# Kernel tuning notes

Measured on AMD Instinct MI355X. Metric: run time of the kernel, lower is better.

Reference implementation:

```python
import jax, jax.numpy as jnp
import numpy as np

# biased_softplus(1.0): bias chosen so softplus(bias) == 1.0 (tensordict NormalParamExtractor default)
_SP_BIAS = float(np.log(np.expm1(1.0)))  # ~0.5413
_SCALE_LB = 1e-4


def setup_inputs() -> dict:
    key = jax.random.key(0)
    ks = jax.random.split(key, 8)
    N, E = 100000, 1600000
    x = jax.random.normal(ks[0], (N, 27), dtype=jnp.float32)
    edge_index = jax.random.randint(ks[1], (2, E), 0, N, dtype=jnp.int64)
    # Linear(27, 64)
    W1 = jax.random.normal(ks[2], (27, 64), dtype=jnp.float32) * 0.1
    b1 = jnp.zeros((64,), dtype=jnp.float32)
    # GraphConv(64, 64): lin_rel (with bias) applied to aggregated neighbors, lin_root (no bias) to self
    Wrel = jax.random.normal(ks[3], (64, 64), dtype=jnp.float32) * 0.1
    brel = jnp.zeros((64,), dtype=jnp.float32)
    Wroot = jax.random.normal(ks[4], (64, 64), dtype=jnp.float32) * 0.1
    # Linear(64, 16)
    W2 = jax.random.normal(ks[5], (64, 16), dtype=jnp.float32) * 0.1
    b2 = jnp.zeros((16,), dtype=jnp.float32)
    return {"x": x, "edge_index": edge_index, "W1": W1, "b1": b1,
            "Wrel": Wrel, "brel": brel, "Wroot": Wroot, "W2": W2, "b2": b2}


def reference(x, edge_index, W1, b1, Wrel, brel, Wroot, W2, b2):
    N = x.shape[0]
    # Linear(27 -> 64)
    h = x @ W1 + b1  # [N, 64]
    # GraphConv: out = lin_rel(sum_{j in N(i)} h_j) + lin_root(h_i)
    src, dst = edge_index[0], edge_index[1]
    agg = jax.ops.segment_sum(h[src], dst, num_segments=N)  # [N, 64]
    h = agg @ Wrel + brel + h @ Wroot
    h = jnp.tanh(h)
    # Linear(64 -> 16) + Tanh
    o = jnp.tanh(h @ W2 + b2)  # [N, 16]
    # NormalParamExtractor: split in half, biased softplus on scale
    loc, raw_scale = jnp.split(o, 2, axis=-1)  # each [N, 8]
    scale = jnp.clip(jax.nn.softplus(raw_scale + _SP_BIAS), _SCALE_LB, None)
    # non-list branch: loc.t().squeeze(-1), scale.t().squeeze(-1)
    return loc.T, scale.T  # each [8, N]
```

## Files before the change

### kernel.cpp

```cpp
#include <hip/hip_runtime.h>
#include <hip/hip_bf16.h>
#include <math.h>

typedef unsigned short ushort_t;
typedef float f32x4 __attribute__((ext_vector_type(4)));
typedef short bf16x8v __attribute__((ext_vector_type(8)));

static constexpr float SP_BIAS = 0.5413248546129181f;
#define LB   512
#define LCAP 12288
#define PCAP 16384
#define MAXB 256
#define CHK  2048
#define BEPB 8192
#define SCAP 96
#define XP   32

__device__ __forceinline__ ushort_t f2bf(float f) {
    union { float f; unsigned u; } v; v.f = f;
    unsigned r = v.u + 0x7FFFu + ((v.u >> 16) & 1u);
    return (ushort_t)(r >> 16);
}
__device__ __forceinline__ float hi2f(unsigned u) {
    union { unsigned u; float f; } v; v.u = u & 0xFFFF0000u;
    return v.f;
}
__device__ __forceinline__ float lo2f(unsigned u) {
    union { unsigned u; float f; } v; v.u = u << 16;
    return v.f;
}

__global__ __launch_bounds__(256) void k_front(
        const int* __restrict__ ei, int* __restrict__ bucketArr,
        int* __restrict__ cellCnt, int E, int NB, int GBIN,
        const float* __restrict__ x, ushort_t* __restrict__ x_bf,
        int N, int GCVT, int* __restrict__ dummyIdx,
        const float* __restrict__ W1, const float* __restrict__ b1,
        const float* __restrict__ Wrel, const float* __restrict__ brel,
        const float* __restrict__ Wroot, const float* __restrict__ W2,
        ushort_t* __restrict__ wF, ushort_t* __restrict__ w2F,
        float* __restrict__ baV, float* __restrict__ bbV) {
    __shared__ alignas(16) char smem[(MAXB + 2 * CHK) * 4];
    __shared__ int s_flag;
    int bid = blockIdx.x, tid = threadIdx.x;
    if (bid < GBIN) {
        int* cursor = (int*)smem;
        int* s_dst  = cursor + MAXB;
        int* s_src  = s_dst + CHK;
        if (tid == 0) s_flag = 0;
        for (int i = tid; i < NB; i += 256) cursor[i] = 0;
        __syncthreads();
        int blk0 = bid * BEPB;
        {
            int cnt0 = E - blk0; if (cnt0 > CHK) cnt0 = CHK;
            int found = 0;
            for (int i = tid; i < cnt0; i += 256) {
                if (ei[2 * (blk0 + i) + 1] != 0) { found = 1; break; }
            }
            if (found) atomicOr(&s_flag, 1);
        }
        __syncthreads();
        int mode32 = s_flag;
        for (int ch = 0; ch < 4; ++ch) {
            int e0 = blk0 + ch * CHK;
            if (e0 >= E) break;
            int cnt = E - e0; if (cnt > CHK) cnt = CHK;
            if (mode32) {
                if ((E & 3) == 0) {
                    const int4* ps = (const int4*)(ei + e0);
                    const int4* pd = (const int4*)(ei + E + e0);
                    int nv = cnt >> 2;
                    for (int i = tid; i < nv; i += 256) {
                        ((int4*)s_src)[i] = ps[i];
                        ((int4*)s_dst)[i] = pd[i];
                    }
                    for (int i = (nv << 2) + tid; i < cnt; i += 256) {
                        s_src[i] = ei[e0 + i];
                        s_dst[i] = ei[E + e0 + i];
                    }
                } else {
                    for (int i = tid; i < cnt; i += 256) {
                        s_src[i] = ei[e0 + i];
                        s_dst[i] = ei[E + e0 + i];
                    }
                }
            } else {
                if ((E & 1) == 0) {
                    const uint4* ps = (const uint4*)ei + (e0 >> 1);
                    const uint4* pd = (const uint4*)ei + ((E + e0) >> 1);
                    int nv = cnt >> 1;
                    for (int i = tid; i < nv; i += 256) {
                        uint4 s = ps[i], d = pd[i];
                        s_src[2 * i] = (int)s.x; s_src[2 * i + 1] = (int)s.z;
                        s_dst[2 * i] = (int)d.x; s_dst[2 * i + 1] = (int)d.z;
                    }
                    if ((cnt & 1) && tid == 0) {
                        s_src[cnt - 1] = ei[2 * (e0 + cnt - 1)];
                        s_dst[cnt - 1] = ei[2 * (E + e0 + cnt - 1)];
                    }
                } else {
                    const int2* p = (const int2*)ei;
                    for (int i = tid; i < cnt; i += 256) {
                        s_src[i] = p[e0 + i].x;
                        s_dst[i] = p[E + e0 + i].x;
                    }
                }
            }
            __syncthreads();
            for (int i = tid; i < cnt; i += 256) {
                int d = s_dst[i];
                int b = d >> 9;
                int pos = atomicAdd(&cursor[b], 1);
                if (pos < SCAP)
                    bucketArr[((size_t)b * GBIN + bid) * SCAP + pos] =
                        ((d & 511) << 17) | s_src[i];
            }
            __syncthreads();
        }
        for (int b = tid; b < NB; b += 256) {
            int cc = cursor[b];
            if (cc > SCAP) cc = SCAP;
            cellCnt[(size_t)bid * NB + b] = cc;
        }
    } else if (bid < GBIN + GCVT) {
        int base = (bid - GBIN) * 64;
        int row = base + (tid >> 2);
        if (row <= N) {
            int c0 = (tid & 3) * 8;
            ushort_t o[8];
#pragma unroll
            for (int c = 0; c < 8; ++c) {
                int col = c0 + c;
                float v = (row < N && col < 27) ? x[(size_t)row * 27 + col] : 0.f;
                o[c] = f2bf(v);
            }
            *(uint4*)(x_bf + (size_t)row * XP + c0) = *(const uint4*)o;
        }
    } else {
        int wb = bid - GBIN - GCVT;
        if (wb < 2) {
            const float* Wr = (wb == 0) ? Wrel : Wroot;
            for (int e = tid; e < 2048; e += 256) {
                int j = e & 7, lane = (e >> 3) & 63, nt = e >> 9;
                int k = ((lane >> 4) << 3) + j;
                int n = (nt << 4) + (lane & 15);
                float v = 0.f;
                if (k < 27) {
                    for (int m = 0; m < 64; ++m)
                        v = fmaf(W1[k * 64 + m], Wr[m * 64 + n], v);
                }
                wF[wb * 2048 + e] = f2bf(v);
            }
        } else {
            for (int e = tid; e < 1024; e += 256) {
                int j = e & 7, lane = (e >> 3) & 63, kt = e >> 9;
                int k = (kt << 5) + ((lane >> 4) << 3) + j;
                int n = (lane & 15);
                w2F[e] = f2bf(W2[k * 16 + n]);
            }
            if (tid < 64) {
                float a = 0.f, b = 0.f;
                for (int m = 0; m < 64; ++m) {
                    a = fmaf(b1[m], Wrel[m * 64 + tid], a);
                    b = fmaf(b1[m], Wroot[m * 64 + tid], b);
                }
                baV[tid] = a;
                bbV[tid] = b + brel[tid];
            }
            if (tid == 255) *dummyIdx = N;
        }
    }
}

__global__ __launch_bounds__(256) void k_local(const int* __restrict__ bucketArr,
                                               const int* __restrict__ cellCnt,
                                               int GBIN, int NB,
                                               int* __restrict__ src_padded,
                                               int* __restrict__ pstart,
                                               int* __restrict__ pdeg,
                                               int* __restrict__ degN,
                                               int N) {
    __shared__ int hist[LB];
    __shared__ int ppos[LB];
    __shared__ int cursor[LB];
    __shared__ int sdata[256];
    __shared__ alignas(16) int spad[LCAP];
    int b = blockIdx.x, tid = threadIdx.x;
    for (int i = tid; i < LB; i += 256) hist[i] = 0;
    __syncthreads();
    const int* arr = bucketArr + (size_t)b * GBIN * SCAP;
    for (int c = tid; c < GBIN; c += 256) {
        const int4* cell4 = (const int4*)(arr + (size_t)c * SCAP);
        int cc = cellCnt[(size_t)c * NB + b];
        int nq = (cc + 3) >> 2;
        for (int q = 0; q < nq; ++q) {
            int4 v = cell4[q];
            int b4 = q * 4;
            if (b4 + 0 < cc) atomicAdd(&hist[v.x >> 17], 1);
            if (b4 + 1 < cc) atomicAdd(&hist[v.y >> 17], 1);
            if (b4 + 2 < cc) atomicAdd(&hist[v.z >> 17], 1);
            if (b4 + 3 < cc) atomicAdd(&hist[v.w >> 17], 1);
        }
    }
    __syncthreads();
    int v0 = hist[2 * tid], v1 = hist[2 * tid + 1];
    int p0 = (v0 + 1) & ~1, p1 = (v1 + 1) & ~1;
    int psum = p0 + p1;
    sdata[tid] = psum;
    __syncthreads();
    for (int off = 1; off < 256; off <<= 1) {
        int add = (tid >= off) ? sdata[tid - off] : 0;
        __syncthreads();
        sdata[tid] += add;
        __syncthreads();
    }
    int pexcl = sdata[tid] - psum;
    ppos[2 * tid] = pexcl;          cursor[2 * tid] = pexcl;
    ppos[2 * tid + 1] = pexcl + p0; cursor[2 * tid + 1] = pexcl + p0;
    __syncthreads();
    int ptot = sdata[255];
    int ptotR = (ptot + 3) & ~3;
    if (ptotR > LCAP) ptotR = LCAP;
    for (int i = tid; i < ptotR; i += 256) spad[i] = N;
    __syncthreads();
    for (int c = tid; c < GBIN; c += 256) {
        const int4* cell4 = (const int4*)(arr + (size_t)c * SCAP);
        int cc = cellCnt[(size_t)c * NB + b];
        int nq = (cc + 3) >> 2;
        for (int q = 0; q < nq; ++q) {
            int4 v = cell4[q];
            int b4 = q * 4;
            int e[4] = {v.x, v.y, v.z, v.w};
#pragma unroll
            for (int r = 0; r < 4; ++r) {
                if (b4 + r < cc) {
                    int pk = e[r];
                    int pos = atomicAdd(&cursor[pk >> 17], 1);
                    if (pos < LCAP) spad[pos] = pk & 0x1FFFF;
                }
            }
        }
    }
    __syncthreads();
    int* outp = src_padded + (size_t)b * PCAP;
    int nt4 = ptotR >> 2;
    for (int i = tid; i < nt4; i += 256)
        ((int4*)outp)[i] = ((const int4*)spad)[i];
    int n0 = b * LB;
    for (int ln = tid; ln < LB; ln += 256) {
        int node = n0 + ln;
        if (node < N) {
            pstart[node] = b * PCAP + ppos[ln];
            pdeg[node] = (hist[ln] + 1) & ~1;
            degN[node] = hist[ln];
        }
    }
}

__global__ __launch_bounds__(256) void k_agg(const ushort_t* __restrict__ x_bf,
                                             const int* __restrict__ src_padded,
                                             const int* __restrict__ pstart,
                                             const int* __restrict__ pdeg,
                                             const int* __restrict__ dummyIdx,
                                             ushort_t* __restrict__ aggx_bf, int N) {
    int w = (blockIdx.x * 256 + threadIdx.x) >> 6;
    int t = threadIdx.x & 63;
    int base = w * 8;
    if (base >= N) return;
    int sub = t >> 3, off = t & 7;
    int node = base + sub;
    int ok = (node < N);
    int st = ok ? pstart[node] : 0;
    int nr = ok ? pdeg[node] : 0;
    const int* ip = src_padded + st;
    int nrmax = nr;
    nrmax = max(nrmax, __shfl_xor(nrmax, 8));
    nrmax = max(nrmax, __shfl_xor(nrmax, 16));
    nrmax = max(nrmax, __shfl_xor(nrmax, 32));
    float a0 = 0.f, a1 = 0.f, a2 = 0.f, a3 = 0.f;
    for (int k = 0; k < nrmax; k += 8) {
        const int* q0 = (k     < nr) ? ip + k     : dummyIdx;
        const int* q1 = (k     < nr) ? ip + k + 1 : dummyIdx;
        const int* q2 = (k + 2 < nr) ? ip + k + 2 : dummyIdx;
        const int* q3 = (k + 2 < nr) ? ip + k + 3 : dummyIdx;
        const int* q4 = (k + 4 < nr) ? ip + k + 4 : dummyIdx;
        const int* q5 = (k + 4 < nr) ? ip + k + 5 : dummyIdx;
        const int* q6 = (k + 6 < nr) ? ip + k + 6 : dummyIdx;
        const int* q7 = (k + 6 < nr) ? ip + k + 7 : dummyIdx;
        int r0 = *q0, r1 = *q1, r2 = *q2, r3 = *q3;
        int r4 = *q4, r5 = *q5, r6 = *q6, r7 = *q7;
        uint2 u0 = *(const uint2*)(x_bf + (size_t)r0 * XP + off * 4);
        uint2 u1 = *(const uint2*)(x_bf + (size_t)r1 * XP + off * 4);
        uint2 u2 = *(const uint2*)(x_bf + (size_t)r2 * XP + off * 4);
        uint2 u3 = *(const uint2*)(x_bf + (size_t)r3 * XP + off * 4);
        uint2 u4 = *(const uint2*)(x_bf + (size_t)r4 * XP + off * 4);
        uint2 u5 = *(const uint2*)(x_bf + (size_t)r5 * XP + off * 4);
        uint2 u6 = *(const uint2*)(x_bf + (size_t)r6 * XP + off * 4);
        uint2 u7 = *(const uint2*)(x_bf + (size_t)r7 * XP + off * 4);
        a0 += lo2f(u0.x); a1 += hi2f(u0.x); a2 += lo2f(u0.y); a3 += hi2f(u0.y);
        a0 += lo2f(u1.x); a1 += hi2f(u1.x); a2 += lo2f(u1.y); a3 += hi2f(u1.y);
        a0 += lo2f(u2.x); a1 += hi2f(u2.x); a2 += lo2f(u2.y); a3 += hi2f(u2.y);
        a0 += lo2f(u3.x); a1 += hi2f(u3.x); a2 += lo2f(u3.y); a3 += hi2f(u3.y);
        a0 += lo2f(u4.x); a1 += hi2f(u4.x); a2 += lo2f(u4.y); a3 += hi2f(u4.y);
        a0 += lo2f(u5.x); a1 += hi2f(u5.x); a2 += lo2f(u5.y); a3 += hi2f(u5.y);
        a0 += lo2f(u6.x); a1 += hi2f(u6.x); a2 += lo2f(u6.y); a3 += hi2f(u6.y);
        a0 += lo2f(u7.x); a1 += hi2f(u7.x); a2 += lo2f(u7.y); a3 += hi2f(u7.y);
    }
    if (ok) {
        uint2 d;
        d.x = ((unsigned)f2bf(a1) << 16) | f2bf(a0);
        d.y = ((unsigned)f2bf(a3) << 16) | f2bf(a2);
        *(uint2*)(aggx_bf + (size_t)node * XP + off * 4) = d;
    }
}

__global__ __launch_bounds__(256) void k_tail(const ushort_t* __restrict__ x_bf,
                                              const ushort_t* __restrict__ aggx_bf,
                                              const int* __restrict__ degN,
                                              const ushort_t* __restrict__ wF_g,
                                              const ushort_t* __restrict__ w2F_g,
                                              const float* __restrict__ baV,
                                              const float* __restrict__ bbV,
                                              const float* __restrict__ b2,
                                              float* __restrict__ out,
                                              int N, int ntiles) {
    __shared__ alignas(16) ushort_t WF[8 * 512];
    __shared__ alignas(16) ushort_t W2F[2 * 512];
    __shared__ alignas(16) ushort_t h2T[4][16 * 72];
    __shared__ float baS[64];
    __shared__ float bbS[64];
    __shared__ float b2S[16];
    int tid = threadIdx.x;
    for (int i = tid; i < 512; i += 256) ((uint4*)WF)[i] = ((const uint4*)wF_g)[i];
    for (int i = tid; i < 128; i += 256) ((uint4*)W2F)[i] = ((const uint4*)w2F_g)[i];
    if (tid < 64) { baS[tid] = baV[tid]; bbS[tid] = bbV[tid]; }
    if (tid < 16) b2S[tid] = b2[tid];
    __syncthreads();

    int lane = tid & 63;
    int wv = tid >> 6;
    int lrow = lane & 15;
    int lkg = lane >> 4;
    const bf16x8v* WFV  = (const bf16x8v*)WF;
    const bf16x8v* W2V  = (const bf16x8v*)W2F;
    ushort_t* myT = h2T[wv];

    for (int tile = blockIdx.x * 4 + wv; tile < ntiles; tile += gridDim.x * 4) {
        int rbase = tile * 16;
        int arow = rbase + lrow; if (arow >= N) arow = N - 1;
        const bf16x8v* aggV = (const bf16x8v*)(aggx_bf + (size_t)arow * XP);
        const bf16x8v* xV   = (const bf16x8v*)(x_bf + (size_t)arow * XP);
        bf16x8v a0 = aggV[lkg];
        bf16x8v a1 = xV[lkg];

        f32x4 acc[4];
#pragma unroll
        for (int nt = 0; nt < 4; ++nt) { acc[nt] = (f32x4){0.f, 0.f, 0.f, 0.f}; }
#pragma unroll
        for (int nt = 0; nt < 4; ++nt) {
            acc[nt] = __builtin_amdgcn_mfma_f32_16x16x32_bf16(a0, WFV[(0 * 4 + nt) * 64 + lane], acc[nt], 0, 0, 0);
            acc[nt] = __builtin_amdgcn_mfma_f32_16x16x32_bf16(a1, WFV[(1 * 4 + nt) * 64 + lane], acc[nt], 0, 0, 0);
        }
        float dgv[4];
#pragma unroll
        for (int r = 0; r < 4; ++r) {
            int node = rbase + lkg * 4 + r;
            dgv[r] = (node < N) ? (float)degN[node] : 0.f;
        }
#pragma unroll
        for (int nt = 0; nt < 4; ++nt) {
            int feat = nt * 16 + lrow;
            float ba = baS[feat], bb = bbS[feat];
#pragma unroll
            for (int r = 0; r < 4; ++r) {
                int noderow = lkg * 4 + r;
                float val = acc[nt][r] + bb + dgv[r] * ba;
                myT[noderow * 72 + feat] = f2bf(tanhf(val));
            }
        }
        __threadfence_block();
        const bf16x8v* h2V = (const bf16x8v*)myT;
        bf16x8v p0 = h2V[lrow * 9 + lkg];
        bf16x8v p1 = h2V[lrow * 9 + 4 + lkg];
        f32x4 acc2 = (f32x4){0.f, 0.f, 0.f, 0.f};
        acc2 = __builtin_amdgcn_mfma_f32_16x16x32_bf16(p0, W2V[0 * 64 + lane], acc2, 0, 0, 0);
        acc2 = __builtin_amdgcn_mfma_f32_16x16x32_bf16(p1, W2V[1 * 64 + lane], acc2, 0, 0, 0);

        int feat = lrow;
        float bias2 = b2S[feat];
#pragma unroll
        for (int r = 0; r < 4; ++r) {
            int node = rbase + lkg * 4 + r;
            float o = tanhf(acc2[r] + bias2);
            if (feat >= 8) {
                float sp = log1pf(expf(o + SP_BIAS));
                o = fmaxf(sp, 1e-4f);
            }
            if (node < N) out[(size_t)feat * N + node] = o;
        }
        __threadfence_block();
    }
}

extern "C" void kernel_launch(void* const* d_in, const int* in_sizes, int n_in,
                              void* d_out, int out_size, void* d_ws, size_t ws_size,
                              hipStream_t stream) {
    const float* x    = (const float*)d_in[0];
    const int*   ei   = (const int*)d_in[1];
    const float* W1   = (const float*)d_in[2];
    const float* b1   = (const float*)d_in[3];
    const float* Wrel = (const float*)d_in[4];
    const float* brel = (const float*)d_in[5];
    const float* Wroot= (const float*)d_in[6];
    const float* W2   = (const float*)d_in[7];
    const float* b2   = (const float*)d_in[8];

    int N = in_sizes[0] / 27;
    int E = in_sizes[1] / 2;

    int NB = (N + LB - 1) / LB;
    int GBIN = (E + BEPB - 1) / BEPB;
    int GCVT = (N + 64) / 64;

    ushort_t* x_bf       = (ushort_t*)d_ws;
    ushort_t* aggx_bf    = x_bf + (size_t)(N + 1) * XP;
    ushort_t* wF_g       = aggx_bf + (size_t)N * XP;
    ushort_t* w2F_g      = wF_g + 4096;
    float*    baV        = (float*)(w2F_g + 1024);
    float*    bbV        = baV + 64;
    int*      bucketArr  = (int*)(bbV + 64);
    int*      cellCnt    = bucketArr + (size_t)NB * GBIN * SCAP;
    int*      src_padded = cellCnt + (size_t)GBIN * NB;
    int*      pstart     = src_padded + (size_t)NB * PCAP;
    int*      pdeg       = pstart + N;
    int*      degN       = pdeg + N;
    int*      dummyIdx   = degN + N;

    int ntiles16 = (N + 15) / 16;

    k_front<<<GBIN + GCVT + 3, 256, 0, stream>>>(
        ei, bucketArr, cellCnt, E, NB, GBIN,
        x, x_bf, N, GCVT, dummyIdx,
        W1, b1, Wrel, brel, Wroot, W2, wF_g, w2F_g, baV, bbV);
    k_local<<<NB, 256, 0, stream>>>(bucketArr, cellCnt, GBIN, NB, src_padded,
                                    pstart, pdeg, degN, N);
    int nwaves8 = (N + 7) / 8;
    k_agg<<<(nwaves8 + 3) / 4, 256, 0, stream>>>(x_bf, src_padded, pstart, pdeg,
                                                 dummyIdx, aggx_bf, N);
    int tgrid = (ntiles16 + 3) / 4; if (tgrid > 1024) tgrid = 1024;
    k_tail<<<tgrid, 256, 0, stream>>>(x_bf, aggx_bf, degN, wF_g, w2F_g,
                                      baV, bbV, b2, (float*)d_out, N, ntiles16);
}
```

Baseline: 80.85 us.

## Stream edges directly into bucket scatter and parallelize cell reads across threads

The binning stage now scatters edges straight from global loads, with no shared-memory staging and no chunk barriers. Each block covers twice as many edges, with larger per-cell capacity, so there are fewer binning blocks. The local sort kernel caches cell counts in shared memory and spreads (cell, quad) work items over all threads, rather than having one thread walk a whole cell serially, which improves load balance and memory parallelism. In exchange, fewer blocks run in the front kernel, bucket storage grows with the larger SCAP, and overflow clipping depends on the new capacity.

Measured after the change: 82.69 us. +2.3%, slower.

```diff
diff --git a/kernel.cpp b/kernel.cpp
--- a/kernel.cpp
+++ b/kernel.cpp
@@ -11,9 +11,9 @@
 #define LCAP 12288
 #define PCAP 16384
 #define MAXB 256
-#define CHK  2048
-#define BEPB 8192
-#define SCAP 96
+#define BEPB 16384
+#define SCAP 160
+#define MAXG 384
 #define XP   32
 
 __device__ __forceinline__ ushort_t f2bf(float f) {
@@ -40,83 +40,67 @@
         const float* __restrict__ Wroot, const float* __restrict__ W2,
         ushort_t* __restrict__ wF, ushort_t* __restrict__ w2F,
         float* __restrict__ baV, float* __restrict__ bbV) {
-    __shared__ alignas(16) char smem[(MAXB + 2 * CHK) * 4];
+    __shared__ int cursor[MAXB];
     __shared__ int s_flag;
     int bid = blockIdx.x, tid = threadIdx.x;
     if (bid < GBIN) {
-        int* cursor = (int*)smem;
-        int* s_dst  = cursor + MAXB;
-        int* s_src  = s_dst + CHK;
         if (tid == 0) s_flag = 0;
         for (int i = tid; i < NB; i += 256) cursor[i] = 0;
         __syncthreads();
         int blk0 = bid * BEPB;
+        int cnt = E - blk0; if (cnt > BEPB) cnt = BEPB;
         {
-            int cnt0 = E - blk0; if (cnt0 > CHK) cnt0 = CHK;
+            int nchk = cnt < 2048 ? cnt : 2048;
             int found = 0;
-            for (int i = tid; i < cnt0; i += 256) {
+            for (int i = tid; i < nchk; i += 256) {
                 if (ei[2 * (blk0 + i) + 1] != 0) { found = 1; break; }
             }
             if (found) atomicOr(&s_flag, 1);
         }
         __syncthreads();
         int mode32 = s_flag;
-        for (int ch = 0; ch < 4; ++ch) {
-            int e0 = blk0 + ch * CHK;
-            if (e0 >= E) break;
-            int cnt = E - e0; if (cnt > CHK) cnt = CHK;
-            if (mode32) {
-                if ((E & 3) == 0) {
-                    const int4* ps = (const int4*)(ei + e0);
-                    const int4* pd = (const int4*)(ei + E + e0);
-                    int nv = cnt >> 2;
-                    for (int i = tid; i < nv; i += 256) {
-                        ((int4*)s_src)[i] = ps[i];
-                        ((int4*)s_dst)[i] = pd[i];
-                    }
-                    for (int i = (nv << 2) + tid; i < cnt; i += 256) {
-                        s_src[i] = ei[e0 + i];
-                        s_dst[i] = ei[E + e0 + i];
-                    }
-                } else {
-                    for (int i = tid; i < cnt; i += 256) {
-                        s_src[i] = ei[e0 + i];
-                        s_dst[i] = ei[E + e0 + i];
-                    }
+        auto scat = [&](int src, int dst) {
+            int b = dst >> 9;
+            int pos = atomicAdd(&cursor[b], 1);
+            if (pos < SCAP)
+                bucketArr[((size_t)b * GBIN + bid) * SCAP + pos] =
+                    ((dst & 511) << 17) | src;
+        };
+        if (mode32) {
+            if ((E & 3) == 0) {
+                const int4* ps = (const int4*)(ei + blk0);
+                const int4* pd = (const int4*)(ei + E + blk0);
+                int nv = cnt >> 2;
+                for (int i = tid; i < nv; i += 256) {
+                    int4 s = ps[i], d = pd[i];
+                    scat(s.x, d.x); scat(s.y, d.y);
+                    scat(s.z, d.z); scat(s.w, d.w);
                 }
+                for (int i = (nv << 2) + tid; i < cnt; i += 256)
+                    scat(ei[blk0 + i], ei[E + blk0 + i]);
             } else {
-                if ((E & 1) == 0) {
-                    const uint4* ps = (const uint4*)ei + (e0 >> 1);
-                    const uint4* pd = (const uint4*)ei + ((E + e0) >> 1);
-                    int nv = cnt >> 1;
-                    for (int i = tid; i < nv; i += 256) {
-                        uint4 s = ps[i], d = pd[i];
-                        s_src[2 * i] = (int)s.x; s_src[2 * i + 1] = (int)s.z;
-                        s_dst[2 * i] = (int)d.x; s_dst[2 * i + 1] = (int)d.z;
-                    }
-                    if ((cnt & 1) && tid == 0) {
-                        s_src[cnt - 1] = ei[2 * (e0 + cnt - 1)];
-                        s_dst[cnt - 1] = ei[2 * (E + e0 + cnt - 1)];
-                    }
-                } else {
-                    const int2* p = (const int2*)ei;
-                    for (int i = tid; i < cnt; i += 256) {
-                        s_src[i] = p[e0 + i].x;
-                        s_dst[i] = p[E + e0 + i].x;
-                    }
+                for (int i = tid; i < cnt; i += 256)
+                    scat(ei[blk0 + i], ei[E + blk0 + i]);
+            }
+        } else {
+            if ((E & 1) == 0) {
+                const uint4* ps = (const uint4*)ei + (blk0 >> 1);
+                const uint4* pd = (const uint4*)ei + ((E + blk0) >> 1);
+                int nv = cnt >> 1;
+                for (int i = tid; i < nv; i += 256) {
+                    uint4 s = ps[i], d = pd[i];
+                    scat((int)s.x, (int)d.x);
+                    scat((int)s.z, (int)d.z);
                 }
-            }
-            __syncthreads();
-            for (int i = tid; i < cnt; i += 256) {
-                int d = s_dst[i];
-                int b = d >> 9;
-                int pos = atomicAdd(&cursor[b], 1);
-                if (pos < SCAP)
-                    bucketArr[((size_t)b * GBIN + bid) * SCAP + pos] =
-                        ((d & 511) << 17) | s_src[i];
-            }
-            __syncthreads();
-        }
+                if ((cnt & 1) && tid == 0)
+                    scat(ei[2 * (blk0 + cnt - 1)], ei[2 * (E + blk0 + cnt - 1)]);
+            } else {
+                const int2* p = (const int2*)ei;
+                for (int i = tid; i < cnt; i += 256)
+                    scat(p[blk0 + i].x, p[E + blk0 + i].x);
+            }
+        }
+        __syncthreads();
         for (int b = tid; b < NB; b += 256) {
             int cc = cursor[b];
             if (cc > SCAP) cc = SCAP;
@@ -184,23 +168,25 @@
     __shared__ int ppos[LB];
     __shared__ int cursor[LB];
     __shared__ int sdata[256];
+    __shared__ int ccnt[MAXG];
     __shared__ alignas(16) int spad[LCAP];
     int b = blockIdx.x, tid = threadIdx.x;
     for (int i = tid; i < LB; i += 256) hist[i] = 0;
+    for (int i = tid; i < GBIN; i += 256) ccnt[i] = cellCnt[(size_t)i * NB + b];
     __syncthreads();
     const int* arr = bucketArr + (size_t)b * GBIN * SCAP;
-    for (int c = tid; c < GBIN; c += 256) {
-        const int4* cell4 = (const int4*)(arr + (size_t)c * SCAP);
-        int cc = cellCnt[(size_t)c * NB + b];
-        int nq = (cc + 3) >> 2;
-        for (int q = 0; q < nq; ++q) {
-            int4 v = cell4[q];
-            int b4 = q * 4;
-            if (b4 + 0 < cc) atomicAdd(&hist[v.x >> 17], 1);
-            if (b4 + 1 < cc) atomicAdd(&hist[v.y >> 17], 1);
-            if (b4 + 2 < cc) atomicAdd(&hist[v.z >> 17], 1);
-            if (b4 + 3 < cc) atomicAdd(&hist[v.w >> 17], 1);
-        }
+    const int QPC = SCAP >> 2;
+    int items = GBIN * QPC;
+    for (int i = tid; i < items; i += 256) {
+        int c = i / QPC, q = i - c * QPC;
+        int cc = ccnt[c];
+        int b4 = q * 4;
+        if (b4 >= cc) continue;
+        int4 v = ((const int4*)(arr + (size_t)c * SCAP))[q];
+        atomicAdd(&hist[v.x >> 17], 1);
+        if (b4 + 1 < cc) atomicAdd(&hist[v.y >> 17], 1);
+        if (b4 + 2 < cc) atomicAdd(&hist[v.z >> 17], 1);
+        if (b4 + 3 < cc) atomicAdd(&hist[v.w >> 17], 1);
     }
     __syncthreads();
     int v0 = hist[2 * tid], v1 = hist[2 * tid + 1];
@@ -223,21 +209,19 @@
     if (ptotR > LCAP) ptotR = LCAP;
     for (int i = tid; i < ptotR; i += 256) spad[i] = N;
     __syncthreads();
-    for (int c = tid; c < GBIN; c += 256) {
-        const int4* cell4 = (const int4*)(arr + (size_t)c * SCAP);
-        int cc = cellCnt[(size_t)c * NB + b];
-        int nq = (cc + 3) >> 2;
-        for (int q = 0; q < nq; ++q) {
-            int4 v = cell4[q];
-            int b4 = q * 4;
-            int e[4] = {v.x, v.y, v.z, v.w};
-#pragma unroll
-            for (int r = 0; r < 4; ++r) {
-                if (b4 + r < cc) {
-                    int pk = e[r];
-                    int pos = atomicAdd(&cursor[pk >> 17], 1);
-                    if (pos < LCAP) spad[pos] = pk & 0x1FFFF;
-                }
+    for (int i = tid; i < items; i += 256) {
+        int c = i / QPC, q = i - c * QPC;
+        int cc = ccnt[c];
+        int b4 = q * 4;
+        if (b4 >= cc) continue;
+        int4 v = ((const int4*)(arr + (size_t)c * SCAP))[q];
+        int e[4] = {v.x, v.y, v.z, v.w};
+#pragma unroll
+        for (int r = 0; r < 4; ++r) {
+            if (b4 + r < cc) {
+                int pk = e[r];
+                int pos = atomicAdd(&cursor[pk >> 17], 1);
+                if (pos < LCAP) spad[pos] = pk & 0x1FFFF;
             }
         }
     }
```

## Fuse local bucket sort with neighbor aggregation, gathering from shared-memory CSR

Applied to the files above, without the earlier changes.

Merges the per-bucket local sort kernel and the aggregation kernel into one. Each block now gathers neighbor features using the source indices it has just placed in shared memory, so it no longer writes and re-reads src_padded, pstart and pdeg in global memory, and one launch goes away. The histogram and scatter loops are also flattened to one work item per cell quad, with cell counts cached in shared memory, and the shared buffer is shrunk. In exchange, the gather phase runs on only about NB (~196) blocks instead of thousands, which may leave too few waves to hide gather latency. The smaller shared-memory capacity also raises the risk of overflow when a bucket is dense.

After: 98.23 us. 1.21x slower.

```diff
diff --git a/kernel.cpp b/kernel.cpp
--- a/kernel.cpp
+++ b/kernel.cpp
@@ -7,14 +7,14 @@
 typedef short bf16x8v __attribute__((ext_vector_type(8)));
 
 static constexpr float SP_BIAS = 0.5413248546129181f;
-#define LB   512
-#define LCAP 12288
-#define PCAP 16384
-#define MAXB 256
-#define CHK  2048
-#define BEPB 8192
-#define SCAP 96
-#define XP   32
+#define LB    512
+#define LCAP2 10240
+#define MAXB  256
+#define CHK   2048
+#define BEPB  8192
+#define SCAP  96
+#define MAXG  256
+#define XP    32
 
 __device__ __forceinline__ ushort_t f2bf(float f) {
     union { float f; unsigned u; } v; v.f = f;
@@ -34,7 +34,7 @@
         const int* __restrict__ ei, int* __restrict__ bucketArr,
         int* __restrict__ cellCnt, int E, int NB, int GBIN,
         const float* __restrict__ x, ushort_t* __restrict__ x_bf,
-        int N, int GCVT, int* __restrict__ dummyIdx,
+        int N, int GCVT,
         const float* __restrict__ W1, const float* __restrict__ b1,
         const float* __restrict__ Wrel, const float* __restrict__ brel,
         const float* __restrict__ Wroot, const float* __restrict__ W2,
@@ -167,40 +167,40 @@
                 baV[tid] = a;
                 bbV[tid] = b + brel[tid];
             }
-            if (tid == 255) *dummyIdx = N;
-        }
-    }
-}
-
-__global__ __launch_bounds__(256) void k_local(const int* __restrict__ bucketArr,
-                                               const int* __restrict__ cellCnt,
-                                               int GBIN, int NB,
-                                               int* __restrict__ src_padded,
-                                               int* __restrict__ pstart,
-                                               int* __restrict__ pdeg,
-                                               int* __restrict__ degN,
-                                               int N) {
+        }
+    }
+}
+
+__global__ __launch_bounds__(256) void k_locagg(const int* __restrict__ bucketArr,
+                                                const int* __restrict__ cellCnt,
+                                                int GBIN, int NB,
+                                                const ushort_t* __restrict__ x_bf,
+                                                ushort_t* __restrict__ aggx_bf,
+                                                int* __restrict__ degN,
+                                                int N) {
     __shared__ int hist[LB];
     __shared__ int ppos[LB];
     __shared__ int cursor[LB];
     __shared__ int sdata[256];
-    __shared__ alignas(16) int spad[LCAP];
+    __shared__ int ccnt[MAXG];
+    __shared__ alignas(16) int spad[LCAP2];
     int b = blockIdx.x, tid = threadIdx.x;
     for (int i = tid; i < LB; i += 256) hist[i] = 0;
+    for (int i = tid; i < GBIN; i += 256) ccnt[i] = cellCnt[(size_t)i * NB + b];
     __syncthreads();
     const int* arr = bucketArr + (size_t)b * GBIN * SCAP;
-    for (int c = tid; c < GBIN; c += 256) {
-        const int4* cell4 = (const int4*)(arr + (size_t)c * SCAP);
-        int cc = cellCnt[(size_t)c * NB + b];
-        int nq = (cc + 3) >> 2;
-        for (int q = 0; q < nq; ++q) {
-            int4 v = cell4[q];
-            int b4 = q * 4;
-            if (b4 + 0 < cc) atomicAdd(&hist[v.x >> 17], 1);
-            if (b4 + 1 < cc) atomicAdd(&hist[v.y >> 17], 1);
-            if (b4 + 2 < cc) atomicAdd(&hist[v.z >> 17], 1);
-            if (b4 + 3 < cc) atomicAdd(&hist[v.w >> 17], 1);
-        }
+    const int QPC = SCAP >> 2;
+    int items = GBIN * QPC;
+    for (int i = tid; i < items; i += 256) {
+        int c = i / QPC, q = i - c * QPC;
+        int cc = ccnt[c];
+        int b4 = q * 4;
+        if (b4 >= cc) continue;
+        int4 v = ((const int4*)(arr + (size_t)c * SCAP))[q];
+        atomicAdd(&hist[v.x >> 17], 1);
+        if (b4 + 1 < cc) atomicAdd(&hist[v.y >> 17], 1);
+        if (b4 + 2 < cc) atomicAdd(&hist[v.z >> 17], 1);
+        if (b4 + 3 < cc) atomicAdd(&hist[v.w >> 17], 1);
     }
     __syncthreads();
     int v0 = hist[2 * tid], v1 = hist[2 * tid + 1];
@@ -220,97 +220,78 @@
     __syncthreads();
     int ptot = sdata[255];
     int ptotR = (ptot + 3) & ~3;
-    if (ptotR > LCAP) ptotR = LCAP;
+    if (ptotR > LCAP2) ptotR = LCAP2;
     for (int i = tid; i < ptotR; i += 256) spad[i] = N;
     __syncthreads();
-    for (int c = tid; c < GBIN; c += 256) {
-        const int4* cell4 = (const int4*)(arr + (size_t)c * SCAP);
-        int cc = cellCnt[(size_t)c * NB + b];
-        int nq = (cc + 3) >> 2;
-        for (int q = 0; q < nq; ++q) {
-            int4 v = cell4[q];
-            int b4 = q * 4;
-            int e[4] = {v.x, v.y, v.z, v.w};
-#pragma unroll
-            for (int r = 0; r < 4; ++r) {
-                if (b4 + r < cc) {
-                    int pk = e[r];
-                    int pos = atomicAdd(&cursor[pk >> 17], 1);
-                    if (pos < LCAP) spad[pos] = pk & 0x1FFFF;
-                }
-            }
-        }
-    }
-    __syncthreads();
-    int* outp = src_padded + (size_t)b * PCAP;
-    int nt4 = ptotR >> 2;
-    for (int i = tid; i < nt4; i += 256)
-        ((int4*)outp)[i] = ((const int4*)spad)[i];
+    for (int i = tid; i < items; i += 256) {
+        int c = i / QPC, q = i - c * QPC;
+        int cc = ccnt[c];
+        int b4 = q * 4;
+        if (b4 >= cc) continue;
+        int4 v = ((const int4*)(arr + (size_t)c * SCAP))[q];
+        int e[4] = {v.x, v.y, v.z, v.w};
+#pragma unroll
+        for (int r = 0; r < 4; ++r) {
+            if (b4 + r < cc) {
+                int pk = e[r];
+                int pos = atomicAdd(&cursor[pk >> 17], 1);
+                if (pos < LCAP2) spad[pos] = pk & 0x1FFFF;
+            }
+        }
+    }
+    __syncthreads();
     int n0 = b * LB;
+    int lane = tid & 63, wv = tid >> 6;
+    int sub = lane >> 3, off = lane & 7;
+    for (int it = 0; it < LB / 32; ++it) {
+        int ln = it * 32 + wv * 8 + sub;
+        int node = n0 + ln;
+        int ok = (node < N);
+        int pp = ppos[ln];
+        int h = hist[ln];
+        int nr = ok ? ((h + 1) & ~1) : 0;
+        int nrmax = nr;
+        nrmax = max(nrmax, __shfl_xor(nrmax, 8));
+        nrmax = max(nrmax, __shfl_xor(nrmax, 16));
+        nrmax = max(nrmax, __shfl_xor(nrmax, 32));
+        float a0 = 0.f, a1 = 0.f, a2 = 0.f, a3 = 0.f;
+        for (int k = 0; k < nrmax; k += 8) {
+            int r0 = (k     < nr) ? spad[pp + k]     : N;
+            int r1 = (k     < nr) ? spad[pp + k + 1] : N;
+            int r2 = (k + 2 < nr) ? spad[pp + k + 2] : N;
+            int r3 = (k + 2 < nr) ? spad[pp + k + 3] : N;
+            int r4 = (k + 4 < nr) ? spad[pp + k + 4] : N;
+            int r5 = (k + 4 < nr) ? spad[pp + k + 5] : N;
+            int r6 = (k + 6 < nr) ? spad[pp + k + 6] : N;
+            int r7 = (k + 6 < nr) ? spad[pp + k + 7] : N;
+            uint2 u0 = *(const uint2*)(x_bf + (size_t)r0 * XP + off * 4);
+            uint2 u1 = *(const uint2*)(x_bf + (size_t)r1 * XP + off * 4);
+            uint2 u2 = *(const uint2*)(x_bf + (size_t)r2 * XP + off * 4);
+            uint2 u3 = *(const uint2*)(x_bf + (size_t)r3 * XP + off * 4);
+            uint2 u4 = *(const uint2*)(x_bf + (size_t)r4 * XP + off * 4);
+            uint2 u5 = *(const uint2*)(x_bf + (size_t)r5 * XP + off * 4);
+            uint2 u6 = *(const uint2*)(x_bf + (size_t)r6 * XP + off * 4);
+            uint2 u7 = *(const uint2*)(x_bf + (size_t)r7 * XP + off * 4);
+            a0 += lo2f(u0.x); a1 += hi2f(u0.x); a2 += lo2f(u0.y); a3 += hi2f(u0.y);
+            a0 += lo2f(u1.x); a1 += hi2f(u1.x); a2 += lo2f(u1.y); a3 += hi2f(u1.y);
+            a0 += lo2f(u2.x); a1 += hi2f(u2.x); a2 += lo2f(u2.y); a3 += hi2f(u2.y);
+            a0 += lo2f(u3.x); a1 += hi2f(u3.x); a2 += lo2f(u3.y); a3 += hi2f(u3.y);
+            a0 += lo2f(u4.x); a1 += hi2f(u4.x); a2 += lo2f(u4.y); a3 += hi2f(u4.y);
+            a0 += lo2f(u5.x); a1 += hi2f(u5.x); a2 += lo2f(u5.y); a3 += hi2f(u5.y);
+            a0 += lo2f(u6.x); a1 += hi2f(u6.x); a2 += lo2f(u6.y); a3 += hi2f(u6.y);
+            a0 += lo2f(u7.x); a1 += hi2f(u7.x); a2 += lo2f(u7.y); a3 += hi2f(u7.y);
+        }
+        if (ok) {
+            uint2 d;
+            d.x = ((unsigned)f2bf(a1) << 16) | f2bf(a0);
+            d.y = ((unsigned)f2bf(a3) << 16) | f2bf(a2);
+            *(uint2*)(aggx_bf + (size_t)node * XP + off * 4) = d;
+            if (lane < 8) {  }
+        }
+    }
     for (int ln = tid; ln < LB; ln += 256) {
         int node = n0 + ln;
-        if (node < N) {
-            pstart[node] = b * PCAP + ppos[ln];
-            pdeg[node] = (hist[ln] + 1) & ~1;
-            degN[node] = hist[ln];
-        }
-    }
-}
-
-__global__ __launch_bounds__(256) void k_agg(const ushort_t* __restrict__ x_bf,
-                                             const int* __restrict__ src_padded,
-                                             const int* __restrict__ pstart,
-                                             const int* __restrict__ pdeg,
-                                             const int* __restrict__ dummyIdx,
-                                             ushort_t* __restrict__ aggx_bf, int N) {
-    int w = (blockIdx.x * 256 + threadIdx.x) >> 6;
-    int t = threadIdx.x & 63;
-    int base = w * 8;
-    if (base >= N) return;
-    int sub = t >> 3, off = t & 7;
-    int node = base + sub;
-    int ok = (node < N);
-    int st = ok ? pstart[node] : 0;
-    int nr = ok ? pdeg[node] : 0;
-    const int* ip = src_padded + st;
-    int nrmax = nr;
-    nrmax = max(nrmax, __shfl_xor(nrmax, 8));
-    nrmax = max(nrmax, __shfl_xor(nrmax, 16));
-    nrmax = max(nrmax, __shfl_xor(nrmax, 32));
-    float a0 = 0.f, a1 = 0.f, a2 = 0.f, a3 = 0.f;
-    for (int k = 0; k < nrmax; k += 8) {
-        const int* q0 = (k     < nr) ? ip + k     : dummyIdx;
-        const int* q1 = (k     < nr) ? ip + k + 1 : dummyIdx;
-        const int* q2 = (k + 2 < nr) ? ip + k + 2 : dummyIdx;
-        const int* q3 = (k + 2 < nr) ? ip + k + 3 : dummyIdx;
-        const int* q4 = (k + 4 < nr) ? ip + k + 4 : dummyIdx;
-        const int* q5 = (k + 4 < nr) ? ip + k + 5 : dummyIdx;
-        const int* q6 = (k + 6 < nr) ? ip + k + 6 : dummyIdx;
-        const int* q7 = (k + 6 < nr) ? ip + k + 7 : dummyIdx;
-        int r0 = *q0, r1 = *q1, r2 = *q2, r3 = *q3;
-        int r4 = *q4, r5 = *q5, r6 = *q6, r7 = *q7;
-        uint2 u0 = *(const uint2*)(x_bf + (size_t)r0 * XP + off * 4);
-        uint2 u1 = *(const uint2*)(x_bf + (size_t)r1 * XP + off * 4);
-        uint2 u2 = *(const uint2*)(x_bf + (size_t)r2 * XP + off * 4);
-        uint2 u3 = *(const uint2*)(x_bf + (size_t)r3 * XP + off * 4);
-        uint2 u4 = *(const uint2*)(x_bf + (size_t)r4 * XP + off * 4);
-        uint2 u5 = *(const uint2*)(x_bf + (size_t)r5 * XP + off * 4);
-        uint2 u6 = *(const uint2*)(x_bf + (size_t)r6 * XP + off * 4);
-        uint2 u7 = *(const uint2*)(x_bf + (size_t)r7 * XP + off * 4);
-        a0 += lo2f(u0.x); a1 += hi2f(u0.x); a2 += lo2f(u0.y); a3 += hi2f(u0.y);
-        a0 += lo2f(u1.x); a1 += hi2f(u1.x); a2 += lo2f(u1.y); a3 += hi2f(u1.y);
-        a0 += lo2f(u2.x); a1 += hi2f(u2.x); a2 += lo2f(u2.y); a3 += hi2f(u2.y);
-        a0 += lo2f(u3.x); a1 += hi2f(u3.x); a2 += lo2f(u3.y); a3 += hi2f(u3.y);
-        a0 += lo2f(u4.x); a1 += hi2f(u4.x); a2 += lo2f(u4.y); a3 += hi2f(u4.y);
-        a0 += lo2f(u5.x); a1 += hi2f(u5.x); a2 += lo2f(u5.y); a3 += hi2f(u5.y);
-        a0 += lo2f(u6.x); a1 += hi2f(u6.x); a2 += lo2f(u6.y); a3 += hi2f(u6.y);
-        a0 += lo2f(u7.x); a1 += hi2f(u7.x); a2 += lo2f(u7.y); a3 += hi2f(u7.y);
-    }
-    if (ok) {
-        uint2 d;
-        d.x = ((unsigned)f2bf(a1) << 16) | f2bf(a0);
-        d.y = ((unsigned)f2bf(a3) << 16) | f2bf(a2);
-        *(uint2*)(aggx_bf + (size_t)node * XP + off * 4) = d;
+        if (node < N) degN[node] = hist[ln];
     }
 }
 
@@ -430,23 +411,16 @@
     float*    bbV        = baV + 64;
     int*      bucketArr  = (int*)(bbV + 64);
     int*      cellCnt    = bucketArr + (size_t)NB * GBIN * SCAP;
-    int*      src_padded = cellCnt + (size_t)GBIN * NB;
-    int*      pstart     = src_padded + (size_t)NB * PCAP;
-    int*      pdeg       = pstart + N;
-    int*      degN       = pdeg + N;
-    int*      dummyIdx   = degN + N;
+    int*      degN       = cellCnt + (size_t)GBIN * NB;
 
     int ntiles16 = (N + 15) / 16;
 
     k_front<<<GBIN + GCVT + 3, 256, 0, stream>>>(
         ei, bucketArr, cellCnt, E, NB, GBIN,
-        x, x_bf, N, GCVT, dummyIdx,
+        x, x_bf, N, GCVT,
         W1, b1, Wrel, brel, Wroot, W2, wF_g, w2F_g, baV, bbV);
-    k_local<<<NB, 256, 0, stream>>>(bucketArr, cellCnt, GBIN, NB, src_padded,
-                                    pstart, pdeg, degN, N);
-    int nwaves8 = (N + 7) / 8;
-    k_agg<<<(nwaves8 + 3) / 4, 256, 0, stream>>>(x_bf, src_padded, pstart, pdeg,
-                                                 dummyIdx, aggx_bf, N);
+    k_locagg<<<NB, 256, 0, stream>>>(bucketArr, cellCnt, GBIN, NB,
+                                     x_bf, aggx_bf, degN, N);
     int tgrid = (ntiles16 + 3) / 4; if (tgrid > 1024) tgrid = 1024;
     k_tail<<<tgrid, 256, 0, stream>>>(x_bf, aggx_bf, degN, wF_g, w2F_g,
                                       baV, bbV, b2, (float*)d_out, N, ntiles16);
```
